# Kernel optimization log

Hardware: AMD Instinct MI355X
Metric: run time of the kernel (lower is better)

The kernel has to match this reference:

```python
import jax, jax.numpy as jnp
import numpy as np

N = 8192       # num_nodes
E = 262144     # num_edges (avg degree 32)
D_IN = 256
D_H = 256
D_OUT = 256
BN_EPS = 1e-5


def _linear_params(key, din, dout):
    # torch nn.Linear default init: U(-1/sqrt(din), 1/sqrt(din))
    s = 1.0 / np.sqrt(din)
    kw, kb = jax.random.split(key)
    W = jax.random.uniform(kw, (dout, din), jnp.float32, -s, s)
    b = jax.random.uniform(kb, (dout,), jnp.float32, -s, s)
    return W, b


def setup_inputs() -> dict:
    key = jax.random.key(0)
    ks = jax.random.split(key, 6)
    x = jax.random.normal(ks[0], (N, D_IN), jnp.float32)
    edge_index = jax.random.randint(ks[1], (2, E), 0, N, dtype=jnp.int64)
    W1, b1 = _linear_params(ks[2], D_IN, D_H)
    W2, b2 = _linear_params(ks[3], D_H, D_H)
    W3, b3 = _linear_params(ks[4], D_H, D_OUT)
    return {
        "x": x, "edge_index": edge_index,
        "W1": W1, "b1": b1, "W2": W2, "b2": b2, "W3": W3, "b3": b3,
        "g1": jnp.ones((D_H,), jnp.float32), "be1": jnp.zeros((D_H,), jnp.float32),
        "g2": jnp.ones((D_H,), jnp.float32), "be2": jnp.zeros((D_H,), jnp.float32),
        "g3": jnp.ones((D_OUT,), jnp.float32), "be3": jnp.zeros((D_OUT,), jnp.float32),
    }


def _build_norm(edge_index):
    # add self loops, scatter 1.0 into dense NxN adjacency (duplicates collapse via set)
    loop = jnp.arange(N, dtype=edge_index.dtype)
    rows = jnp.concatenate([edge_index[0], loop])
    cols = jnp.concatenate([edge_index[1], loop])
    adj = jnp.zeros((N, N), jnp.float32).at[rows, cols].set(1.0)
    deg = adj.sum(axis=1)
    dinv = jnp.where(deg > 0, deg ** -0.5, 0.0)  # inf -> 0 as in original
    return dinv[:, None] * adj * dinv[None, :]


def _gcn(x, norm, W, b):
    # linear then symmetric-normalized aggregation
    return norm @ (x @ W.T + b)


def _bn(x, g, b):
    # BatchNorm1d with batch statistics (biased var), eps=1e-5
    mu = x.mean(axis=0)
    var = x.var(axis=0)
    return (x - mu) * jax.lax.rsqrt(var + BN_EPS) * g + b


def reference(x, edge_index, W1, b1, W2, b2, W3, b3, g1, be1, g2, be2, g3, be3):
    norm = _build_norm(edge_index)
    h = jax.nn.relu(_bn(_gcn(x, norm, W1, b1), g1, be1))
    h = jax.nn.relu(_bn(_gcn(h, norm, W2, b2), g2, be2))
    h = _bn(_gcn(h, norm, W3, b3), g3, be3)
    return h
```

## Files before the change

### kernel.cpp

```cpp
#include <hip/hip_runtime.h>

#define N_NODES 8192
#define N_EDGES 262144
#define D 256
#define ADJ_WORDS 256
#define MAX_DEG 128
#define AGG_BLOCKS 2048
#define NPART 16

typedef __attribute__((ext_vector_type(8))) short bf16x8;
typedef __attribute__((ext_vector_type(4))) float f32x4;

__device__ __forceinline__ short f2bf(float f) {
    unsigned u = __builtin_bit_cast(unsigned, f);
    u += 0x7fffu + ((u >> 16) & 1);
    return (short)(u >> 16);
}
__device__ __forceinline__ float bf2f(unsigned short u) {
    return __builtin_bit_cast(float, ((unsigned)u) << 16);
}

__global__ __launch_bounds__(256) void build_adj(const int* __restrict__ ei,
                                                 unsigned* __restrict__ adj,
                                                 int* __restrict__ deg,
                                                 const float* __restrict__ W1,
                                                 const float* __restrict__ W2,
                                                 const float* __restrict__ W3,
                                                 unsigned short* __restrict__ Wb1,
                                                 unsigned short* __restrict__ Wb2,
                                                 unsigned short* __restrict__ Wb3) {
    int i = blockIdx.x * 256 + threadIdx.x;
    if (i >= N_EDGES + N_NODES) {
        int j = i - (N_EDGES + N_NODES);
        int which = j >> 16, k = j & 65535;
        const float* src = which == 0 ? W1 : which == 1 ? W2 : W3;
        unsigned short* dst = which == 0 ? Wb1 : which == 1 ? Wb2 : Wb3;
        dst[k] = (unsigned short)f2bf(src[k]);
        return;
    }
    int r, c;
    if (i < N_EDGES) {
        r = ei[i];
        c = ei[N_EDGES + i];
    } else {
        r = i - N_EDGES;
        c = r;
    }
    unsigned bit = 1u << (c & 31);
    unsigned old = atomicOr(&adj[r * ADJ_WORDS + (c >> 5)], bit);
    if (!(old & bit)) atomicAdd(&deg[r], 1);
}

__device__ __forceinline__ void nbrs_body(const unsigned* __restrict__ adj,
                                          const int* __restrict__ deg,
                                          int* __restrict__ nbr_idx,
                                          float* __restrict__ nbr_w, int r) {
    const int t = threadIdx.x;
    const int lane = t & 63, wave = t >> 6;
    unsigned m = adj[r * ADJ_WORDS + t];
    int cnt = __popc(m);
    int x = cnt;
    #pragma unroll
    for (int off = 1; off < 64; off <<= 1) {
        int v = __shfl_up(x, off, 64);
        if (lane >= off) x += v;
    }
    __shared__ int wtot[4];
    if (lane == 63) wtot[wave] = x;
    __syncthreads();
    int woff = 0;
    #pragma unroll
    for (int w = 0; w < 4; w++) woff += (w < wave) ? wtot[w] : 0;
    int base = woff + x - cnt;
    const float dr = rsqrtf((float)deg[r]);
    int* oi = nbr_idx + (size_t)r * MAX_DEG;
    float* ow = nbr_w + (size_t)r * MAX_DEG;
    while (m) {
        int b = __ffs(m) - 1;
        m &= m - 1;
        int c = (t << 5) + b;
        if (base < MAX_DEG) {
            oi[base] = c;
            ow[base] = dr * rsqrtf((float)deg[c]);
        }
        base++;
    }
}

template <bool APPLY, bool RELU>
__device__ __forceinline__ void gemm_body(const float* __restrict__ Xsrc,
                                          const float* __restrict__ psA,
                                          const float* __restrict__ psQ,
                                          const float* __restrict__ g,
                                          const float* __restrict__ be,
                                          const unsigned short* __restrict__ Wb,
                                          const float* __restrict__ bias,
                                          unsigned short* __restrict__ Hb,
                                          int bn, int bm) {
    __shared__ float ssc[256], ssh[256];
    const int tid = threadIdx.x;
    if (APPLY) {
        float s = 0.f, q = 0.f;
        #pragma unroll
        for (int i = 0; i < NPART; i++) {
            s += psA[i * 256 + tid];
            q += psQ[i * 256 + tid];
        }
        float mu = s * (1.0f / N_NODES);
        float var = q * (1.0f / N_NODES) - mu * mu;
        float rstd = rsqrtf(var + 1e-5f);
        float sc = g[tid] * rstd;
        ssc[tid] = sc;
        ssh[tid] = be[tid] - mu * sc;
        __syncthreads();
    }

    const int wave = tid >> 6, lane = tid & 63;
    const int l16 = lane & 15, q = lane >> 4;
    const int mrow0 = bm + wave * 32;

    f32x4 acc[2][4];
    #pragma unroll
    for (int i = 0; i < 2; i++)
        #pragma unroll
        for (int j = 0; j < 4; j++) acc[i][j] = (f32x4){0.f, 0.f, 0.f, 0.f};

    for (int k0 = 0; k0 < D; k0 += 32) {
        const int kq = k0 + q * 8;
        bf16x8 xb[2];
        float4 sc0, sc1, sh0, sh1;
        if (APPLY) {
            sc0 = *(const float4*)(ssc + kq);
            sc1 = *(const float4*)(ssc + kq + 4);
            sh0 = *(const float4*)(ssh + kq);
            sh1 = *(const float4*)(ssh + kq + 4);
        }
        #pragma unroll
        for (int mf = 0; mf < 2; mf++) {
            const float* xr = Xsrc + (size_t)(mrow0 + mf * 16 + l16) * D + kq;
            float4 a = *(const float4*)xr;
            float4 b = *(const float4*)(xr + 4);
            float v[8] = {a.x, a.y, a.z, a.w, b.x, b.y, b.z, b.w};
            if (APPLY) {
                float sc[8] = {sc0.x, sc0.y, sc0.z, sc0.w, sc1.x, sc1.y, sc1.z, sc1.w};
                float sh[8] = {sh0.x, sh0.y, sh0.z, sh0.w, sh1.x, sh1.y, sh1.z, sh1.w};
                #pragma unroll
                for (int j = 0; j < 8; j++) {
                    v[j] = fmaf(v[j], sc[j], sh[j]);
                    if (RELU) v[j] = fmaxf(v[j], 0.0f);
                }
            }
            #pragma unroll
            for (int j = 0; j < 8; j++) xb[mf][j] = f2bf(v[j]);
        }
        #pragma unroll
        for (int nf = 0; nf < 4; nf++) {
            bf16x8 wa = *(const bf16x8*)(Wb + (size_t)(bn + nf * 16 + l16) * D + kq);
            #pragma unroll
            for (int mf = 0; mf < 2; mf++)
                acc[mf][nf] = __builtin_amdgcn_mfma_f32_16x16x32_bf16(wa, xb[mf], acc[mf][nf], 0, 0, 0);
        }
    }

    #pragma unroll
    for (int mf = 0; mf < 2; mf++) {
        const int m = mrow0 + mf * 16 + l16;
        #pragma unroll
        for (int nf = 0; nf < 4; nf++) {
            const int nb = bn + nf * 16 + q * 4;
            float4 b4 = *(const float4*)(bias + nb);
            short4 o;
            o.x = f2bf(acc[mf][nf][0] + b4.x);
            o.y = f2bf(acc[mf][nf][1] + b4.y);
            o.z = f2bf(acc[mf][nf][2] + b4.z);
            o.w = f2bf(acc[mf][nf][3] + b4.w);
            *(short4*)(Hb + (size_t)m * D + nb) = o;
        }
    }
}

__global__ __launch_bounds__(256) void gemm1_and_nbrs(const float* __restrict__ x,
                                                      const unsigned short* __restrict__ Wb1,
                                                      const float* __restrict__ b1,
                                                      unsigned short* __restrict__ Hb,
                                                      const unsigned* __restrict__ adj,
                                                      const int* __restrict__ deg,
                                                      int* __restrict__ nbr_idx,
                                                      float* __restrict__ nbr_w) {
    const int bg = blockIdx.x;
    if (bg < 256) {
        gemm_body<false, false>(x, nullptr, nullptr, nullptr, nullptr, Wb1, b1, Hb,
                                (bg & 3) * 64, (bg >> 2) * 128);
    } else {
        nbrs_body(adj, deg, nbr_idx, nbr_w, bg - 256);
    }
}

__global__ __launch_bounds__(256) void gemm_mfma_bn(const float* __restrict__ Xsrc,
                                                    const float* __restrict__ psA,
                                                    const float* __restrict__ psQ,
                                                    const float* __restrict__ g,
                                                    const float* __restrict__ be,
                                                    const unsigned short* __restrict__ Wb,
                                                    const float* __restrict__ bias,
                                                    unsigned short* __restrict__ Hb) {
    gemm_body<true, true>(Xsrc, psA, psQ, g, be, Wb, bias, Hb,
                          blockIdx.x * 64, blockIdx.y * 128);
}

__global__ __launch_bounds__(256) void aggregate_bf16(const int* __restrict__ nbr_idx,
                                                      const float* __restrict__ nbr_w,
                                                      const int* __restrict__ deg,
                                                      const unsigned short* __restrict__ Hb,
                                                      float* __restrict__ G,
                                                      float* __restrict__ psA,
                                                      float* __restrict__ psQ) {
    const int wave = threadIdx.x >> 6;
    const int lane = threadIdx.x & 63;
    const int ch = lane * 4;
    const int r = blockIdx.x * 4 + wave;

    int dg = deg[r]; if (dg > MAX_DEG) dg = MAX_DEG;
    const int* idx = nbr_idx + (size_t)r * MAX_DEG;
    const float* wt = nbr_w + (size_t)r * MAX_DEG;
    float4 A = make_float4(0.f, 0.f, 0.f, 0.f);
    int j = 0;
    for (; j + 8 <= dg; j += 8) {
        int4 c0 = *(const int4*)(idx + j);
        int4 c1 = *(const int4*)(idx + j + 4);
        float4 w0 = *(const float4*)(wt + j);
        float4 w1 = *(const float4*)(wt + j + 4);
        ushort4 u0 = *(const ushort4*)(Hb + (size_t)c0.x * D + ch);
        ushort4 u1 = *(const ushort4*)(Hb + (size_t)c0.y * D + ch);
        ushort4 u2 = *(const ushort4*)(Hb + (size_t)c0.z * D + ch);
        ushort4 u3 = *(const ushort4*)(Hb + (size_t)c0.w * D + ch);
        ushort4 u4 = *(const ushort4*)(Hb + (size_t)c1.x * D + ch);
        ushort4 u5 = *(const ushort4*)(Hb + (size_t)c1.y * D + ch);
        ushort4 u6 = *(const ushort4*)(Hb + (size_t)c1.z * D + ch);
        ushort4 u7 = *(const ushort4*)(Hb + (size_t)c1.w * D + ch);
        A.x = fmaf(w0.x, bf2f(u0.x), A.x); A.y = fmaf(w0.x, bf2f(u0.y), A.y);
        A.z = fmaf(w0.x, bf2f(u0.z), A.z); A.w = fmaf(w0.x, bf2f(u0.w), A.w);
        A.x = fmaf(w0.y, bf2f(u1.x), A.x); A.y = fmaf(w0.y, bf2f(u1.y), A.y);
        A.z = fmaf(w0.y, bf2f(u1.z), A.z); A.w = fmaf(w0.y, bf2f(u1.w), A.w);
        A.x = fmaf(w0.z, bf2f(u2.x), A.x); A.y = fmaf(w0.z, bf2f(u2.y), A.y);
        A.z = fmaf(w0.z, bf2f(u2.z), A.z); A.w = fmaf(w0.z, bf2f(u2.w), A.w);
        A.x = fmaf(w0.w, bf2f(u3.x), A.x); A.y = fmaf(w0.w, bf2f(u3.y), A.y);
        A.z = fmaf(w0.w, bf2f(u3.z), A.z); A.w = fmaf(w0.w, bf2f(u3.w), A.w);
        A.x = fmaf(w1.x, bf2f(u4.x), A.x); A.y = fmaf(w1.x, bf2f(u4.y), A.y);
        A.z = fmaf(w1.x, bf2f(u4.z), A.z); A.w = fmaf(w1.x, bf2f(u4.w), A.w);
        A.x = fmaf(w1.y, bf2f(u5.x), A.x); A.y = fmaf(w1.y, bf2f(u5.y), A.y);
        A.z = fmaf(w1.y, bf2f(u5.z), A.z); A.w = fmaf(w1.y, bf2f(u5.w), A.w);
        A.x = fmaf(w1.z, bf2f(u6.x), A.x); A.y = fmaf(w1.z, bf2f(u6.y), A.y);
        A.z = fmaf(w1.z, bf2f(u6.z), A.z); A.w = fmaf(w1.z, bf2f(u6.w), A.w);
        A.x = fmaf(w1.w, bf2f(u7.x), A.x); A.y = fmaf(w1.w, bf2f(u7.y), A.y);
        A.z = fmaf(w1.w, bf2f(u7.z), A.z); A.w = fmaf(w1.w, bf2f(u7.w), A.w);
    }
    for (; j + 4 <= dg; j += 4) {
        int4 c0 = *(const int4*)(idx + j);
        float4 w0 = *(const float4*)(wt + j);
        ushort4 u0 = *(const ushort4*)(Hb + (size_t)c0.x * D + ch);
        ushort4 u1 = *(const ushort4*)(Hb + (size_t)c0.y * D + ch);
        ushort4 u2 = *(const ushort4*)(Hb + (size_t)c0.z * D + ch);
        ushort4 u3 = *(const ushort4*)(Hb + (size_t)c0.w * D + ch);
        A.x = fmaf(w0.x, bf2f(u0.x), A.x); A.y = fmaf(w0.x, bf2f(u0.y), A.y);
        A.z = fmaf(w0.x, bf2f(u0.z), A.z); A.w = fmaf(w0.x, bf2f(u0.w), A.w);
        A.x = fmaf(w0.y, bf2f(u1.x), A.x); A.y = fmaf(w0.y, bf2f(u1.y), A.y);
        A.z = fmaf(w0.y, bf2f(u1.z), A.z); A.w = fmaf(w0.y, bf2f(u1.w), A.w);
        A.x = fmaf(w0.z, bf2f(u2.x), A.x); A.y = fmaf(w0.z, bf2f(u2.y), A.y);
        A.z = fmaf(w0.z, bf2f(u2.z), A.z); A.w = fmaf(w0.z, bf2f(u2.w), A.w);
        A.x = fmaf(w0.w, bf2f(u3.x), A.x); A.y = fmaf(w0.w, bf2f(u3.y), A.y);
        A.z = fmaf(w0.w, bf2f(u3.z), A.z); A.w = fmaf(w0.w, bf2f(u3.w), A.w);
    }
    for (; j < dg; j++) {
        int c = idx[j];
        float w = wt[j];
        ushort4 u = *(const ushort4*)(Hb + (size_t)c * D + ch);
        A.x = fmaf(w, bf2f(u.x), A.x); A.y = fmaf(w, bf2f(u.y), A.y);
        A.z = fmaf(w, bf2f(u.z), A.z); A.w = fmaf(w, bf2f(u.w), A.w);
    }
    *(float4*)(G + (size_t)r * D + ch) = A;

    __shared__ float ls[4][256], lss[4][256];
    ls[wave][ch] = A.x; ls[wave][ch + 1] = A.y; ls[wave][ch + 2] = A.z; ls[wave][ch + 3] = A.w;
    lss[wave][ch] = A.x * A.x; lss[wave][ch + 1] = A.y * A.y;
    lss[wave][ch + 2] = A.z * A.z; lss[wave][ch + 3] = A.w * A.w;
    __syncthreads();
    const int t = threadIdx.x;
    const int prow = (blockIdx.x & (NPART - 1)) * 256;
    atomicAdd(&psA[prow + t], ls[0][t] + ls[1][t] + ls[2][t] + ls[3][t]);
    atomicAdd(&psQ[prow + t], lss[0][t] + lss[1][t] + lss[2][t] + lss[3][t]);
}

__global__ __launch_bounds__(256) void bn_apply_out(const float* __restrict__ G,
                                                    const float* __restrict__ psA,
                                                    const float* __restrict__ psQ,
                                                    const float* __restrict__ g,
                                                    const float* __restrict__ be,
                                                    float* __restrict__ Out) {
    __shared__ float ssc[256], ssh[256];
    const int tid = threadIdx.x;
    {
        float s = 0.f, q = 0.f;
        #pragma unroll
        for (int i = 0; i < NPART; i++) {
            s += psA[i * 256 + tid];
            q += psQ[i * 256 + tid];
        }
        float mu = s * (1.0f / N_NODES);
        float var = q * (1.0f / N_NODES) - mu * mu;
        float rstd = rsqrtf(var + 1e-5f);
        float sc = g[tid] * rstd;
        ssc[tid] = sc;
        ssh[tid] = be[tid] - mu * sc;
        __syncthreads();
    }
    const int rows_per_block = 64;
    const int r0 = blockIdx.x * rows_per_block;
    const int ch = (tid & 63) * 4;
    const int rsub = tid >> 6;
    float4 sc = *(const float4*)(ssc + ch);
    float4 sh = *(const float4*)(ssh + ch);
    for (int rr = rsub; rr < rows_per_block; rr += 4) {
        const size_t off = (size_t)(r0 + rr) * D + ch;
        float4 v = *(const float4*)(G + off);
        v.x = fmaf(v.x, sc.x, sh.x);
        v.y = fmaf(v.y, sc.y, sh.y);
        v.z = fmaf(v.z, sc.z, sh.z);
        v.w = fmaf(v.w, sc.w, sh.w);
        *(float4*)(Out + off) = v;
    }
}

extern "C" void kernel_launch(void* const* d_in, const int* in_sizes, int n_in,
                              void* d_out, int out_size, void* d_ws, size_t ws_size,
                              hipStream_t stream) {
    const float* x  = (const float*)d_in[0];
    const int*   ei = (const int*)d_in[1];
    const float* W1 = (const float*)d_in[2];
    const float* b1 = (const float*)d_in[3];
    const float* W2 = (const float*)d_in[4];
    const float* b2 = (const float*)d_in[5];
    const float* W3 = (const float*)d_in[6];
    const float* b3 = (const float*)d_in[7];
    const float* g1 = (const float*)d_in[8];
    const float* be1 = (const float*)d_in[9];
    const float* g2 = (const float*)d_in[10];
    const float* be2 = (const float*)d_in[11];
    const float* g3 = (const float*)d_in[12];
    const float* be3 = (const float*)d_in[13];

    char* ws = (char*)d_ws;
    unsigned*       adj  = (unsigned*)ws;
    int*            deg  = (int*)(ws + (8 << 20));
    float*          psA0 = (float*)(ws + (8 << 20) + (32 << 10));
    float*          psQ0 = psA0 + NPART * 256;
    float*          psA1 = psQ0 + NPART * 256;
    float*          psQ1 = psA1 + NPART * 256;
    float*          psA2 = psQ1 + NPART * 256;
    float*          psQ2 = psA2 + NPART * 256;
    unsigned short* Wb1  = (unsigned short*)(ws + (8 << 20) + (128 << 10));
    unsigned short* Wb2  = (unsigned short*)(ws + (8 << 20) + (256 << 10));
    unsigned short* Wb3  = (unsigned short*)(ws + (8 << 20) + (384 << 10));
    int*            nbr_idx = (int*)  (ws + (9 << 20));
    float*          nbr_w   = (float*)(ws + (13 << 20));
    float*          G       = (float*)(ws + (17 << 20));
    unsigned short* Hb      = (unsigned short*)(ws + (25 << 20));

    hipMemsetAsync(ws, 0, (8 << 20) + (128 << 10), stream);

    build_adj<<<1824, 256, 0, stream>>>(ei, adj, deg, W1, W2, W3, Wb1, Wb2, Wb3);

    gemm1_and_nbrs<<<256 + N_NODES, 256, 0, stream>>>(x, Wb1, b1, Hb, adj, deg, nbr_idx, nbr_w);
    aggregate_bf16<<<AGG_BLOCKS, 256, 0, stream>>>(nbr_idx, nbr_w, deg, Hb, G, psA0, psQ0);

    dim3 ggrid(D / 64, N_NODES / 128);

    gemm_mfma_bn<<<ggrid, 256, 0, stream>>>(G, psA0, psQ0, g1, be1, Wb2, b2, Hb);
    aggregate_bf16<<<AGG_BLOCKS, 256, 0, stream>>>(nbr_idx, nbr_w, deg, Hb, G, psA1, psQ1);

    gemm_mfma_bn<<<ggrid, 256, 0, stream>>>(G, psA1, psQ1, g2, be2, Wb3, b3, Hb);
    aggregate_bf16<<<AGG_BLOCKS, 256, 0, stream>>>(nbr_idx, nbr_w, deg, Hb, G, psA2, psQ2);

    bn_apply_out<<<N_NODES / 64, 256, 0, stream>>>(G, psA2, psQ2, g3, be3, (float*)d_out);
}
```

Baseline: 226.9 us.

## Factor symmetric degree normalization out of aggregation and widen gather loads

Splits the edge weight dinv[r]*dinv[c] into a column scale applied in the GEMM epilogue (scaling H rows by dinv) and a row scale applied after aggregation. This removes the per-edge weight array, its writes in the neighbor-list build and its reads during aggregation, so the inner loop becomes plain adds. Aggregation is also restructured so each half-wave handles alternate neighbors with 16-byte loads of 8 channels, then combines the halves with a cross-lane shuffle. Scaling H by dinv before the bf16 rounding changes the rounding slightly.

```diff
diff --git a/kernel.cpp b/kernel.cpp
--- a/kernel.cpp
+++ b/kernel.cpp
@@ -9,6 +9,7 @@
 #define NPART 16
 
 typedef __attribute__((ext_vector_type(8))) short bf16x8;
+typedef __attribute__((ext_vector_type(8))) unsigned short u16x8;
 typedef __attribute__((ext_vector_type(4))) float f32x4;
 
 __device__ __forceinline__ short f2bf(float f) {
@@ -52,9 +53,7 @@
 }
 
 __device__ __forceinline__ void nbrs_body(const unsigned* __restrict__ adj,
-                                          const int* __restrict__ deg,
-                                          int* __restrict__ nbr_idx,
-                                          float* __restrict__ nbr_w, int r) {
+                                          int* __restrict__ nbr_idx, int r) {
     const int t = threadIdx.x;
     const int lane = t & 63, wave = t >> 6;
     unsigned m = adj[r * ADJ_WORDS + t];
@@ -72,17 +71,12 @@
     #pragma unroll
     for (int w = 0; w < 4; w++) woff += (w < wave) ? wtot[w] : 0;
     int base = woff + x - cnt;
-    const float dr = rsqrtf((float)deg[r]);
     int* oi = nbr_idx + (size_t)r * MAX_DEG;
-    float* ow = nbr_w + (size_t)r * MAX_DEG;
     while (m) {
         int b = __ffs(m) - 1;
         m &= m - 1;
         int c = (t << 5) + b;
-        if (base < MAX_DEG) {
-            oi[base] = c;
-            ow[base] = dr * rsqrtf((float)deg[c]);
-        }
+        if (base < MAX_DEG) oi[base] = c;
         base++;
     }
 }
@@ -95,6 +89,7 @@
                                           const float* __restrict__ be,
                                           const unsigned short* __restrict__ Wb,
                                           const float* __restrict__ bias,
+                                          const int* __restrict__ deg,
                                           unsigned short* __restrict__ Hb,
                                           int bn, int bm) {
     __shared__ float ssc[256], ssh[256];
@@ -165,15 +160,16 @@
     #pragma unroll
     for (int mf = 0; mf < 2; mf++) {
         const int m = mrow0 + mf * 16 + l16;
+        const float di = rsqrtf((float)deg[m]);
         #pragma unroll
         for (int nf = 0; nf < 4; nf++) {
             const int nb = bn + nf * 16 + q * 4;
             float4 b4 = *(const float4*)(bias + nb);
             short4 o;
-            o.x = f2bf(acc[mf][nf][0] + b4.x);
-            o.y = f2bf(acc[mf][nf][1] + b4.y);
-            o.z = f2bf(acc[mf][nf][2] + b4.z);
-            o.w = f2bf(acc[mf][nf][3] + b4.w);
+            o.x = f2bf((acc[mf][nf][0] + b4.x) * di);
+            o.y = f2bf((acc[mf][nf][1] + b4.y) * di);
+            o.z = f2bf((acc[mf][nf][2] + b4.z) * di);
+            o.w = f2bf((acc[mf][nf][3] + b4.w) * di);
             *(short4*)(Hb + (size_t)m * D + nb) = o;
         }
     }
@@ -182,17 +178,16 @@
 __global__ __launch_bounds__(256) void gemm1_and_nbrs(const float* __restrict__ x,
                                                       const unsigned short* __restrict__ Wb1,
                                                       const float* __restrict__ b1,
+                                                      const int* __restrict__ deg,
                                                       unsigned short* __restrict__ Hb,
                                                       const unsigned* __restrict__ adj,
-                                                      const int* __restrict__ deg,
-                                                      int* __restrict__ nbr_idx,
-                                                      float* __restrict__ nbr_w) {
+                                                      int* __restrict__ nbr_idx) {
     const int bg = blockIdx.x;
     if (bg < 256) {
-        gemm_body<false, false>(x, nullptr, nullptr, nullptr, nullptr, Wb1, b1, Hb,
+        gemm_body<false, false>(x, nullptr, nullptr, nullptr, nullptr, Wb1, b1, deg, Hb,
                                 (bg & 3) * 64, (bg >> 2) * 128);
     } else {
-        nbrs_body(adj, deg, nbr_idx, nbr_w, bg - 256);
+        nbrs_body(adj, nbr_idx, bg - 256);
     }
 }
 
@@ -203,13 +198,13 @@
                                                     const float* __restrict__ be,
                                                     const unsigned short* __restrict__ Wb,
                                                     const float* __restrict__ bias,
+                                                    const int* __restrict__ deg,
                                                     unsigned short* __restrict__ Hb) {
-    gemm_body<true, true>(Xsrc, psA, psQ, g, be, Wb, bias, Hb,
+    gemm_body<true, true>(Xsrc, psA, psQ, g, be, Wb, bias, deg, Hb,
                           blockIdx.x * 64, blockIdx.y * 128);
 }
 
 __global__ __launch_bounds__(256) void aggregate_bf16(const int* __restrict__ nbr_idx,
-                                                      const float* __restrict__ nbr_w,
                                                       const int* __restrict__ deg,
                                                       const unsigned short* __restrict__ Hb,
                                                       float* __restrict__ G,
@@ -217,73 +212,85 @@
                                                       float* __restrict__ psQ) {
     const int wave = threadIdx.x >> 6;
     const int lane = threadIdx.x & 63;
-    const int ch = lane * 4;
+    const int half = lane >> 5;
+    const int l32 = lane & 31;
+    const int ch = l32 * 8;
     const int r = blockIdx.x * 4 + wave;
 
-    int dg = deg[r]; if (dg > MAX_DEG) dg = MAX_DEG;
+    const int dgr = deg[r];
+    int dg = dgr; if (dg > MAX_DEG) dg = MAX_DEG;
     const int* idx = nbr_idx + (size_t)r * MAX_DEG;
-    const float* wt = nbr_w + (size_t)r * MAX_DEG;
-    float4 A = make_float4(0.f, 0.f, 0.f, 0.f);
-    int j = 0;
-    for (; j + 8 <= dg; j += 8) {
-        int4 c0 = *(const int4*)(idx + j);
-        int4 c1 = *(const int4*)(idx + j + 4);
-        float4 w0 = *(const float4*)(wt + j);
-        float4 w1 = *(const float4*)(wt + j + 4);
-        ushort4 u0 = *(const ushort4*)(Hb + (size_t)c0.x * D + ch);
-        ushort4 u1 = *(const ushort4*)(Hb + (size_t)c0.y * D + ch);
-        ushort4 u2 = *(const ushort4*)(Hb + (size_t)c0.z * D + ch);
-        ushort4 u3 = *(const ushort4*)(Hb + (size_t)c0.w * D + ch);
-        ushort4 u4 = *(const ushort4*)(Hb + (size_t)c1.x * D + ch);
-        ushort4 u5 = *(const ushort4*)(Hb + (size_t)c1.y * D + ch);
-        ushort4 u6 = *(const ushort4*)(Hb + (size_t)c1.z * D + ch);
-        ushort4 u7 = *(const ushort4*)(Hb + (size_t)c1.w * D + ch);
-        A.x = fmaf(w0.x, bf2f(u0.x), A.x); A.y = fmaf(w0.x, bf2f(u0.y), A.y);
-        A.z = fmaf(w0.x, bf2f(u0.z), A.z); A.w = fmaf(w0.x, bf2f(u0.w), A.w);
-        A.x = fmaf(w0.y, bf2f(u1.x), A.x); A.y = fmaf(w0.y, bf2f(u1.y), A.y);
-        A.z = fmaf(w0.y, bf2f(u1.z), A.z); A.w = fmaf(w0.y, bf2f(u1.w), A.w);
-        A.x = fmaf(w0.z, bf2f(u2.x), A.x); A.y = fmaf(w0.z, bf2f(u2.y), A.y);
-        A.z = fmaf(w0.z, bf2f(u2.z), A.z); A.w = fmaf(w0.z, bf2f(u2.w), A.w);
-        A.x = fmaf(w0.w, bf2f(u3.x), A.x); A.y = fmaf(w0.w, bf2f(u3.y), A.y);
-        A.z = fmaf(w0.w, bf2f(u3.z), A.z); A.w = fmaf(w0.w, bf2f(u3.w), A.w);
-        A.x = fmaf(w1.x, bf2f(u4.x), A.x); A.y = fmaf(w1.x, bf2f(u4.y), A.y);
-        A.z = fmaf(w1.x, bf2f(u4.z), A.z); A.w = fmaf(w1.x, bf2f(u4.w), A.w);
-        A.x = fmaf(w1.y, bf2f(u5.x), A.x); A.y = fmaf(w1.y, bf2f(u5.y), A.y);
-        A.z = fmaf(w1.y, bf2f(u5.z), A.z); A.w = fmaf(w1.y, bf2f(u5.w), A.w);
-        A.x = fmaf(w1.z, bf2f(u6.x), A.x); A.y = fmaf(w1.z, bf2f(u6.y), A.y);
-        A.z = fmaf(w1.z, bf2f(u6.z), A.z); A.w = fmaf(w1.z, bf2f(u6.w), A.w);
-        A.x = fmaf(w1.w, bf2f(u7.x), A.x); A.y = fmaf(w1.w, bf2f(u7.y), A.y);
-        A.z = fmaf(w1.w, bf2f(u7.z), A.z); A.w = fmaf(w1.w, bf2f(u7.w), A.w);
-    }
-    for (; j + 4 <= dg; j += 4) {
-        int4 c0 = *(const int4*)(idx + j);
-        float4 w0 = *(const float4*)(wt + j);
-        ushort4 u0 = *(const ushort4*)(Hb + (size_t)c0.x * D + ch);
-        ushort4 u1 = *(const ushort4*)(Hb + (size_t)c0.y * D + ch);
-        ushort4 u2 = *(const ushort4*)(Hb + (size_t)c0.z * D + ch);
-        ushort4 u3 = *(const ushort4*)(Hb + (size_t)c0.w * D + ch);
-        A.x = fmaf(w0.x, bf2f(u0.x), A.x); A.y = fmaf(w0.x, bf2f(u0.y), A.y);
-        A.z = fmaf(w0.x, bf2f(u0.z), A.z); A.w = fmaf(w0.x, bf2f(u0.w), A.w);
-        A.x = fmaf(w0.y, bf2f(u1.x), A.x); A.y = fmaf(w0.y, bf2f(u1.y), A.y);
-        A.z = fmaf(w0.y, bf2f(u1.z), A.z); A.w = fmaf(w0.y, bf2f(u1.w), A.w);
-        A.x = fmaf(w0.z, bf2f(u2.x), A.x); A.y = fmaf(w0.z, bf2f(u2.y), A.y);
-        A.z = fmaf(w0.z, bf2f(u2.z), A.z); A.w = fmaf(w0.z, bf2f(u2.w), A.w);
-        A.x = fmaf(w0.w, bf2f(u3.x), A.x); A.y = fmaf(w0.w, bf2f(u3.y), A.y);
-        A.z = fmaf(w0.w, bf2f(u3.z), A.z); A.w = fmaf(w0.w, bf2f(u3.w), A.w);
-    }
-    for (; j < dg; j++) {
+    const unsigned short* hb = Hb + ch;
+
+    float A[8] = {0.f, 0.f, 0.f, 0.f, 0.f, 0.f, 0.f, 0.f};
+    int base = 0;
+    for (; base + 16 <= dg; base += 16) {
+        const int* p = idx + base + half;
+        int c0 = p[0], c1 = p[2], c2 = p[4], c3 = p[6];
+        int c4 = p[8], c5 = p[10], c6 = p[12], c7 = p[14];
+        u16x8 u0 = *(const u16x8*)(hb + (size_t)c0 * D);
+        u16x8 u1 = *(const u16x8*)(hb + (size_t)c1 * D);
+        u16x8 u2 = *(const u16x8*)(hb + (size_t)c2 * D);
+        u16x8 u3 = *(const u16x8*)(hb + (size_t)c3 * D);
+        u16x8 u4 = *(const u16x8*)(hb + (size_t)c4 * D);
+        u16x8 u5 = *(const u16x8*)(hb + (size_t)c5 * D);
+        u16x8 u6 = *(const u16x8*)(hb + (size_t)c6 * D);
+        u16x8 u7 = *(const u16x8*)(hb + (size_t)c7 * D);
+        #pragma unroll
+        for (int i = 0; i < 8; i++) A[i] += bf2f(u0[i]);
+        #pragma unroll
+        for (int i = 0; i < 8; i++) A[i] += bf2f(u1[i]);
+        #pragma unroll
+        for (int i = 0; i < 8; i++) A[i] += bf2f(u2[i]);
+        #pragma unroll
+        for (int i = 0; i < 8; i++) A[i] += bf2f(u3[i]);
+        #pragma unroll
+        for (int i = 0; i < 8; i++) A[i] += bf2f(u4[i]);
+        #pragma unroll
+        for (int i = 0; i < 8; i++) A[i] += bf2f(u5[i]);
+        #pragma unroll
+        for (int i = 0; i < 8; i++) A[i] += bf2f(u6[i]);
+        #pragma unroll
+        for (int i = 0; i < 8; i++) A[i] += bf2f(u7[i]);
+    }
+    for (; base + 8 <= dg; base += 8) {
+        const int* p = idx + base + half;
+        int c0 = p[0], c1 = p[2], c2 = p[4], c3 = p[6];
+        u16x8 u0 = *(const u16x8*)(hb + (size_t)c0 * D);
+        u16x8 u1 = *(const u16x8*)(hb + (size_t)c1 * D);
+        u16x8 u2 = *(const u16x8*)(hb + (size_t)c2 * D);
+        u16x8 u3 = *(const u16x8*)(hb + (size_t)c3 * D);
+        #pragma unroll
+        for (int i = 0; i < 8; i++) A[i] += bf2f(u0[i]);
+        #pragma unroll
+        for (int i = 0; i < 8; i++) A[i] += bf2f(u1[i]);
+        #pragma unroll
+        for (int i = 0; i < 8; i++) A[i] += bf2f(u2[i]);
+        #pragma unroll
+        for (int i = 0; i < 8; i++) A[i] += bf2f(u3[i]);
+    }
+    for (int j = base + half; j < dg; j += 2) {
         int c = idx[j];
-        float w = wt[j];
-        ushort4 u = *(const ushort4*)(Hb + (size_t)c * D + ch);
-        A.x = fmaf(w, bf2f(u.x), A.x); A.y = fmaf(w, bf2f(u.y), A.y);
-        A.z = fmaf(w, bf2f(u.z), A.z); A.w = fmaf(w, bf2f(u.w), A.w);
-    }
-    *(float4*)(G + (size_t)r * D + ch) = A;
+        u16x8 u = *(const u16x8*)(hb + (size_t)c * D);
+        #pragma unroll
+        for (int i = 0; i < 8; i++) A[i] += bf2f(u[i]);
+    }
+
+    const float dr = rsqrtf((float)dgr);
+    #pragma unroll
+    for (int i = 0; i < 8; i++) A[i] += __shfl_xor(A[i], 32, 64);
+    const int cp = ch + half * 4;
+    float4 o;
+    o.x = A[half * 4 + 0] * dr;
+    o.y = A[half * 4 + 1] * dr;
+    o.z = A[half * 4 + 2] * dr;
+    o.w = A[half * 4 + 3] * dr;
+    *(float4*)(G + (size_t)r * D + cp) = o;
 
     __shared__ float ls[4][256], lss[4][256];
-    ls[wave][ch] = A.x; ls[wave][ch + 1] = A.y; ls[wave][ch + 2] = A.z; ls[wave][ch + 3] = A.w;
-    lss[wave][ch] = A.x * A.x; lss[wave][ch + 1] = A.y * A.y;
-    lss[wave][ch + 2] = A.z * A.z; lss[wave][ch + 3] = A.w * A.w;
+    ls[wave][cp] = o.x; ls[wave][cp + 1] = o.y; ls[wave][cp + 2] = o.z; ls[wave][cp + 3] = o.w;
+    lss[wave][cp] = o.x * o.x; lss[wave][cp + 1] = o.y * o.y;
+    lss[wave][cp + 2] = o.z * o.z; lss[wave][cp + 3] = o.w * o.w;
     __syncthreads();
     const int t = threadIdx.x;
     const int prow = (blockIdx.x & (NPART - 1)) * 256;
@@ -362,24 +369,23 @@
     unsigned short* Wb2  = (unsigned short*)(ws + (8 << 20) + (256 << 10));
     unsigned short* Wb3  = (unsigned short*)(ws + (8 << 20) + (384 << 10));
     int*            nbr_idx = (int*)  (ws + (9 << 20));
-    float*          nbr_w   = (float*)(ws + (13 << 20));
-    float*          G       = (float*)(ws + (17 << 20));
-    unsigned short* Hb      = (unsigned short*)(ws + (25 << 20));
+    float*          G       = (float*)(ws + (13 << 20));
+    unsigned short* Hb      = (unsigned short*)(ws + (21 << 20));
 
     hipMemsetAsync(ws, 0, (8 << 20) + (128 << 10), stream);
 
     build_adj<<<1824, 256, 0, stream>>>(ei, adj, deg, W1, W2, W3, Wb1, Wb2, Wb3);
 
-    gemm1_and_nbrs<<<256 + N_NODES, 256, 0, stream>>>(x, Wb1, b1, Hb, adj, deg, nbr_idx, nbr_w);
-    aggregate_bf16<<<AGG_BLOCKS, 256, 0, stream>>>(nbr_idx, nbr_w, deg, Hb, G, psA0, psQ0);
+    gemm1_and_nbrs<<<256 + N_NODES, 256, 0, stream>>>(x, Wb1, b1, deg, Hb, adj, nbr_idx);
+    aggregate_bf16<<<AGG_BLOCKS, 256, 0, stream>>>(nbr_idx, deg, Hb, G, psA0, psQ0);
 
     dim3 ggrid(D / 64, N_NODES / 128);
 
-    gemm_mfma_bn<<<ggrid, 256, 0, stream>>>(G, psA0, psQ0, g1, be1, Wb2, b2, Hb);
-    aggregate_bf16<<<AGG_BLOCKS, 256, 0, stream>>>(nbr_idx, nbr_w, deg, Hb, G, psA1, psQ1);
-
-    gemm_mfma_bn<<<ggrid, 256, 0, stream>>>(G, psA1, psQ1, g2, be2, Wb3, b3, Hb);
-    aggregate_bf16<<<AGG_BLOCKS, 256, 0, stream>>>(nbr_idx, nbr_w, deg, Hb, G, psA2, psQ2);
+    gemm_mfma_bn<<<ggrid, 256, 0, stream>>>(G, psA0, psQ0, g1, be1, Wb2, b2, deg, Hb);
+    aggregate_bf16<<<AGG_BLOCKS, 256, 0, stream>>>(nbr_idx, deg, Hb, G, psA1, psQ1);
+
+    gemm_mfma_bn<<<ggrid, 256, 0, stream>>>(G, psA1, psQ1, g2, be2, Wb3, b3, deg, Hb);
+    aggregate_bf16<<<AGG_BLOCKS, 256, 0, stream>>>(nbr_idx, deg, Hb, G, psA2, psQ2);
 
     bn_apply_out<<<N_NODES / 64, 256, 0, stream>>>(G, psA2, psQ2, g3, be3, (float*)d_out);
 }
```

Result: faster. 215.7 us (-4.9%).
